# Kernel tuning notes

Hardware: AMD Instinct MI355X
Metric: run time of the kernel (lower is better)

Reference implementation:

```python
import jax, jax.numpy as jnp
import numpy as np

B, T, IN, H, L, P = 512, 512, 1, 100, 4, 0.5  # batch, seq, input, hidden, layers, dropout


def setup_inputs() -> dict:
    key = jax.random.key(0)
    ks = jax.random.split(key, 12)
    k = 1.0 / np.sqrt(H)  # torch nn.LSTM init scale
    u = lambda kk, shape: jax.random.uniform(kk, shape, jnp.float32, -k, k)
    inp = {
        "x": jax.random.normal(ks[0], (B, T, IN), jnp.float32),
        "W_ih0": u(ks[1], (4 * H, IN)),          # layer 0 input weights
        "W_ih_rest": u(ks[2], (L - 1, 4 * H, H)),  # layers 1..3 input weights
        "W_hh": u(ks[3], (L, 4 * H, H)),
        "b_ih": u(ks[4], (L, 4 * H)),
        "b_hh": u(ks[5], (L, 4 * H)),
        "W_out": u(ks[6], (1, H)),
        "b_out": u(ks[7], (1,)),
        # inter-layer dropout keep-masks (torch applies dropout to outputs of layers 0..L-2)
        "drop_masks": jax.random.bernoulli(ks[8], 1.0 - P, (L - 1, B, T, H)).astype(jnp.float32),
    }
    return inp


def _lstm_layer(seq, Wih, Whh, b):
    # seq: [T, B, in_dim]; returns [T, B, H]. PyTorch gate order: i, f, g, o.
    h0 = jnp.zeros((seq.shape[1], Whh.shape[-1]), seq.dtype)

    def step(carry, xt):
        h, c = carry
        gates = xt @ Wih.T + h @ Whh.T + b  # [B, 4H]
        i, f, g, o = jnp.split(gates, 4, axis=-1)
        c = jax.nn.sigmoid(f) * c + jax.nn.sigmoid(i) * jnp.tanh(g)
        h = jax.nn.sigmoid(o) * jnp.tanh(c)
        return (h, c), h

    _, hs = jax.lax.scan(step, (h0, h0), seq)
    return hs


def reference(x, W_ih0, W_ih_rest, W_hh, b_ih, b_hh, W_out, b_out, drop_masks):
    scale = 1.0 / (1.0 - P)
    seq = jnp.swapaxes(x, 0, 1)  # [T, B, IN] (batch_first -> time-major)
    seq = _lstm_layer(seq, W_ih0, W_hh[0], b_ih[0] + b_hh[0])
    for l in range(1, L):
        seq = seq * (jnp.swapaxes(drop_masks[l - 1], 0, 1) * scale)
        seq = _lstm_layer(seq, W_ih_rest[l - 1], W_hh[l], b_ih[l] + b_hh[l])
    last = seq[-1]  # [B, H] == lstm_out[:, -1]
    return last @ W_out.T + b_out  # [B, 1]
```

## Files before the change

kernel.cpp:

```cpp
#include <hip/hip_runtime.h>
#include <cstdint>
#include <cstddef>

#define BB 512
#define TT 512
#define HH 100
#define G4 400

template<bool IS_L0, bool WRITE_DROP>
__global__ __launch_bounds__(448, 2)
void rec_kernel(const float* __restrict__ x,
                const float* __restrict__ xc,
                const float* __restrict__ Whh_l,
                const float* __restrict__ Wih0,
                const float* __restrict__ bih_l,
                const float* __restrict__ bhh_l,
                const float* __restrict__ dmask_l,
                float* __restrict__ hdrop,
                float* __restrict__ st_h,
                float* __restrict__ st_c)
{
    __shared__ float hbuf[2][2][112];
    __shared__ float gsh[2][400];

    const int tid = threadIdx.x;
    const int p   = tid >> 1;
    const int e   = tid & 1;
    const bool rowok = (p < 200);
    const int pc  = rowok ? p : 199;
    const int r0  = pc;
    const int r1  = pc + 200;
    const int b   = blockIdx.x * 2 + e;

    float wf0[100], wf1[100];
    {
        const float4* w0 = (const float4*)(Whh_l + (size_t)r0 * HH);
        const float4* w1 = (const float4*)(Whh_l + (size_t)r1 * HH);
        #pragma unroll
        for (int m = 0; m < 25; ++m) {
            ((float4*)wf0)[m] = w0[m];
            ((float4*)wf1)[m] = w1[m];
        }
    }

    float wx0 = 0.f, wx1 = 0.f, bs0 = 0.f, bs1 = 0.f;
    if (IS_L0) {
        wx0 = Wih0[r0];  bs0 = bih_l[r0] + bhh_l[r0];
        wx1 = Wih0[r1];  bs1 = bih_l[r1] + bhh_l[r1];
    }

    ((float*)hbuf)[tid] = 0.f;

    const bool p2 = (p < HH);
    const int jj  = p2 ? p : 0;
    float c2 = 0.f, hlast = 0.f;

    __syncthreads();

    float gin0 = 0.f, gin1 = 0.f, xv = 0.f, mk = 0.f;
    if (IS_L0) {
        xv = x[(size_t)b * TT];
    } else {
        gin0 = xc[(size_t)b * G4 + r0];
        gin1 = xc[(size_t)b * G4 + r1];
    }
    if (WRITE_DROP && p2) mk = dmask_l[(size_t)b * TT * HH + jj];

    int cur = 0;
    for (int t = 0; t < TT; ++t) {
        const int tn = (t + 1 < TT) ? (t + 1) : t;

        float nxv = 0.f, ngin0 = 0.f, ngin1 = 0.f, nmk = 0.f;
        if (IS_L0) {
            nxv = x[(size_t)b * TT + tn];
        } else {
            const size_t base = (size_t)tn * BB * G4 + (size_t)b * G4;
            ngin0 = xc[base + r0];
            ngin1 = xc[base + r1];
        }
        if (WRITE_DROP && p2) nmk = dmask_l[((size_t)b * TT + tn) * HH + jj];

        if (IS_L0) {
            gin0 = fmaf(xv, wx0, bs0);
            gin1 = fmaf(xv, wx1, bs1);
        }

        float a0 = 0.f, a0b = 0.f, a1 = 0.f, a1b = 0.f;
        {
            const float4* hp = (const float4*)&hbuf[cur][e][0];
            #pragma unroll
            for (int m = 0; m < 25; ++m) {
                const float4 hv = hp[m];
                a0  = fmaf(wf0[4 * m + 0], hv.x, a0);
                a0b = fmaf(wf0[4 * m + 1], hv.y, a0b);
                a0  = fmaf(wf0[4 * m + 2], hv.z, a0);
                a0b = fmaf(wf0[4 * m + 3], hv.w, a0b);
                a1  = fmaf(wf1[4 * m + 0], hv.x, a1);
                a1b = fmaf(wf1[4 * m + 1], hv.y, a1b);
                a1  = fmaf(wf1[4 * m + 2], hv.z, a1);
                a1b = fmaf(wf1[4 * m + 3], hv.w, a1b);
            }
        }
        if (rowok) {
            gsh[e][pc]       = a0 + a0b + gin0;
            gsh[e][pc + 200] = a1 + a1b + gin1;
        }
        __syncthreads();

        const int nxt = cur ^ 1;
        if (p2) {
            const float gi = gsh[e][jj];
            const float gf = gsh[e][HH + jj];
            const float gg = gsh[e][2 * HH + jj];
            const float go = gsh[e][3 * HH + jj];
            const float i_ = 1.f / (1.f + __expf(-gi));
            const float f_ = 1.f / (1.f + __expf(-gf));
            const float o_ = 1.f / (1.f + __expf(-go));
            const float gt = 1.f - 2.f / (__expf(gg + gg) + 1.f);
            c2 = fmaf(f_, c2, i_ * gt);
            const float th = 1.f - 2.f / (__expf(c2 + c2) + 1.f);
            const float h = o_ * th;
            hlast = h;
            hbuf[nxt][e][jj] = h;
            if (WRITE_DROP)
                hdrop[((size_t)t * BB + b) * HH + jj] = h * mk * 2.f;
        }
        __syncthreads();
        cur = nxt;
        gin0 = ngin0; gin1 = ngin1;
        xv = nxv; mk = nmk;
    }

    if (p2) {
        st_h[(size_t)b * HH + jj] = hlast;
        st_c[(size_t)b * HH + jj] = c2;
    }
}

__global__ __launch_bounds__(256, 2)
void xc_gemm(const float* __restrict__ A,
             const float* __restrict__ W,
             const float* __restrict__ bih_l,
             const float* __restrict__ bhh_l,
             float* __restrict__ xc)
{
    __shared__ float At[HH][132];
    __shared__ float Bt[HH][68];

    const int tid = threadIdx.x;
    const int n0  = blockIdx.x * 64;
    const size_t m0 = (size_t)blockIdx.y * 128;

    for (int s = tid; s < 128 * 25; s += 256) {
        const int r = s / 25, kq = s - r * 25;
        const float4 v = *(const float4*)&A[(m0 + r) * HH + kq * 4];
        At[kq * 4 + 0][r] = v.x; At[kq * 4 + 1][r] = v.y;
        At[kq * 4 + 2][r] = v.z; At[kq * 4 + 3][r] = v.w;
    }
    for (int s = tid; s < 64 * 25; s += 256) {
        const int r = s / 25, kq = s - r * 25;
        const int col = n0 + r;
        float4 v = {0.f, 0.f, 0.f, 0.f};
        if (col < G4) v = *(const float4*)&W[(size_t)col * HH + kq * 4];
        Bt[kq * 4 + 0][r] = v.x; Bt[kq * 4 + 1][r] = v.y;
        Bt[kq * 4 + 2][r] = v.z; Bt[kq * 4 + 3][r] = v.w;
    }
    __syncthreads();

    const int tx = tid & 15;
    const int ty = tid >> 4;
    float acc[8][4];
    #pragma unroll
    for (int i = 0; i < 8; ++i)
        #pragma unroll
        for (int j = 0; j < 4; ++j) acc[i][j] = 0.f;

    #pragma unroll 4
    for (int k = 0; k < HH; ++k) {
        const float4 a0 = *(const float4*)&At[k][ty * 8];
        const float4 a1 = *(const float4*)&At[k][ty * 8 + 4];
        const float4 bv = *(const float4*)&Bt[k][tx * 4];
        const float av[8] = {a0.x, a0.y, a0.z, a0.w, a1.x, a1.y, a1.z, a1.w};
        #pragma unroll
        for (int i = 0; i < 8; ++i) {
            acc[i][0] = fmaf(av[i], bv.x, acc[i][0]);
            acc[i][1] = fmaf(av[i], bv.y, acc[i][1]);
            acc[i][2] = fmaf(av[i], bv.z, acc[i][2]);
            acc[i][3] = fmaf(av[i], bv.w, acc[i][3]);
        }
    }

    const int col = n0 + tx * 4;
    if (col < G4) {
        const float4 u = *(const float4*)&bih_l[col];
        const float4 v = *(const float4*)&bhh_l[col];
        const float4 bias = {u.x + v.x, u.y + v.y, u.z + v.z, u.w + v.w};
        #pragma unroll
        for (int i = 0; i < 8; ++i) {
            const size_t r = m0 + ty * 8 + i;
            float4 o = {acc[i][0] + bias.x, acc[i][1] + bias.y,
                        acc[i][2] + bias.z, acc[i][3] + bias.w};
            *(float4*)&xc[r * G4 + col] = o;
        }
    }
}

__global__ __launch_bounds__(256)
void out_kernel(const float* __restrict__ st_h3,
                const float* __restrict__ Wout,
                const float* __restrict__ bout,
                float* __restrict__ out)
{
    const int b = blockIdx.x * 256 + threadIdx.x;
    if (b < BB) {
        float sum = bout[0];
        #pragma unroll 4
        for (int k = 0; k < HH; ++k)
            sum = fmaf(st_h3[(size_t)b * HH + k], Wout[k], sum);
        out[b] = sum;
    }
}

extern "C" void kernel_launch(void* const* d_in, const int* in_sizes, int n_in,
                              void* d_out, int out_size, void* d_ws, size_t ws_size,
                              hipStream_t stream)
{
    const float* x     = (const float*)d_in[0];
    const float* Wih0  = (const float*)d_in[1];
    const float* WihR  = (const float*)d_in[2];
    const float* Whh   = (const float*)d_in[3];
    const float* bih   = (const float*)d_in[4];
    const float* bhh   = (const float*)d_in[5];
    const float* Wout  = (const float*)d_in[6];
    const float* bout  = (const float*)d_in[7];
    const float* dmask = (const float*)d_in[8];
    float* out = (float*)d_out;

    float* ws    = (float*)d_ws;
    float* xcb   = ws;
    float* hdrop = xcb + (size_t)TT * BB * G4;
    float* sth   = hdrop + (size_t)TT * BB * HH;
    float* stc   = sth + (size_t)4 * BB * HH;

    const dim3 rgrid(BB / 2), rblk(448);
    const dim3 ggrid(7, (TT * BB) / 128), gblk(256);

    rec_kernel<true, true><<<rgrid, rblk, 0, stream>>>(
        x, nullptr, Whh, Wih0, bih, bhh, dmask,
        hdrop, sth, stc);
    for (int l = 1; l < 4; ++l) {
        xc_gemm<<<ggrid, gblk, 0, stream>>>(
            hdrop, WihR + (size_t)(l - 1) * G4 * HH,
            bih + l * G4, bhh + l * G4, xcb);
        if (l < 3) {
            rec_kernel<false, true><<<rgrid, rblk, 0, stream>>>(
                nullptr, xcb, Whh + (size_t)l * G4 * HH,
                nullptr, nullptr, nullptr,
                dmask + (size_t)l * BB * TT * HH,
                hdrop, sth + (size_t)l * BB * HH, stc + (size_t)l * BB * HH);
        } else {
            rec_kernel<false, false><<<rgrid, rblk, 0, stream>>>(
                nullptr, xcb, Whh + (size_t)l * G4 * HH,
                nullptr, nullptr, nullptr,
                nullptr,
                nullptr, sth + (size_t)l * BB * HH, stc + (size_t)l * BB * HH);
        }
    }
    out_kernel<<<dim3(2), dim3(256), 0, stream>>>(sth + (size_t)3 * BB * HH, Wout, bout, out);
}
```

Measured before the change: 4.155 ms.

## Rework recurrent kernel activations and widen xc GEMM tile to 128x128

The recurrent kernel now stages the W_hh matrix through a 160KB shared buffer so the per-thread weight loads are coalesced, and drops its occupancy hint to one block per CU. It also moves gate activations (sigmoid, and tanh for the g gate) into the GEMV threads, so the cell-update threads only compute c and h. The input GEMM switches to a 128x128 tile with an 8x8 per-thread micro-tile and scalar staging loads, using fewer column blocks. The large shared allocation limits residency to one block per CU, and the scalar GEMM loads may coalesce less well.

After: 5.920 ms. 1.42x slower.

```diff
diff --git a/kernel.cpp b/kernel.cpp
--- a/kernel.cpp
+++ b/kernel.cpp
@@ -8,7 +8,7 @@
 #define G4 400
 
 template<bool IS_L0, bool WRITE_DROP>
-__global__ __launch_bounds__(448, 2)
+__global__ __launch_bounds__(448, 1)
 void rec_kernel(const float* __restrict__ x,
                 const float* __restrict__ xc,
                 const float* __restrict__ Whh_l,
@@ -20,8 +20,7 @@
                 float* __restrict__ st_h,
                 float* __restrict__ st_c)
 {
-    __shared__ float hbuf[2][2][112];
-    __shared__ float gsh[2][400];
+    __shared__ float sh[G4 * HH];
 
     const int tid = threadIdx.x;
     const int p   = tid >> 1;
@@ -32,16 +31,25 @@
     const int r1  = pc + 200;
     const int b   = blockIdx.x * 2 + e;
 
-    float wf0[100], wf1[100];
     {
-        const float4* w0 = (const float4*)(Whh_l + (size_t)r0 * HH);
-        const float4* w1 = (const float4*)(Whh_l + (size_t)r1 * HH);
+        const float4* src = (const float4*)Whh_l;
+        float4* dst = (float4*)sh;
+        for (int i = tid; i < G4 * HH / 4; i += 448) dst[i] = src[i];
+    }
+    __syncthreads();
+
+    float4 wf0[25], wf1[25];
+    {
+        const float4* s0 = (const float4*)&sh[r0 * HH];
+        const float4* s1 = (const float4*)&sh[r1 * HH];
         #pragma unroll
-        for (int m = 0; m < 25; ++m) {
-            ((float4*)wf0)[m] = w0[m];
-            ((float4*)wf1)[m] = w1[m];
-        }
-    }
+        for (int m = 0; m < 25; ++m) { wf0[m] = s0[m]; wf1[m] = s1[m]; }
+    }
+    __syncthreads();
+
+    for (int i = tid; i < G4 * HH; i += 448) sh[i] = 0.f;
+
+    float* gshp = sh + 448;
 
     float wx0 = 0.f, wx1 = 0.f, bs0 = 0.f, bs1 = 0.f;
     if (IS_L0) {
@@ -49,10 +57,9 @@
         wx1 = Wih0[r1];  bs1 = bih_l[r1] + bhh_l[r1];
     }
 
-    ((float*)hbuf)[tid] = 0.f;
-
-    const bool p2 = (p < HH);
-    const int jj  = p2 ? p : 0;
+    const bool isP2 = (tid < 200);
+    const int jj  = p;
+    const bool sel = (p < HH);
     float c2 = 0.f, hlast = 0.f;
 
     __syncthreads();
@@ -64,7 +71,7 @@
         gin0 = xc[(size_t)b * G4 + r0];
         gin1 = xc[(size_t)b * G4 + r1];
     }
-    if (WRITE_DROP && p2) mk = dmask_l[(size_t)b * TT * HH + jj];
+    if (WRITE_DROP && isP2) mk = dmask_l[(size_t)b * TT * HH + jj];
 
     int cur = 0;
     for (int t = 0; t < TT; ++t) {
@@ -74,11 +81,11 @@
         if (IS_L0) {
             nxv = x[(size_t)b * TT + tn];
         } else {
-            const size_t base = (size_t)tn * BB * G4 + (size_t)b * G4;
+            const size_t base = (size_t)tn * (BB * G4) + (size_t)b * G4;
             ngin0 = xc[base + r0];
             ngin1 = xc[base + r1];
         }
-        if (WRITE_DROP && p2) nmk = dmask_l[((size_t)b * TT + tn) * HH + jj];
+        if (WRITE_DROP && isP2) nmk = dmask_l[((size_t)b * TT + tn) * HH + jj];
 
         if (IS_L0) {
             gin0 = fmaf(xv, wx0, bs0);
@@ -87,57 +94,60 @@
 
         float a0 = 0.f, a0b = 0.f, a1 = 0.f, a1b = 0.f;
         {
-            const float4* hp = (const float4*)&hbuf[cur][e][0];
+            const float4* hp = (const float4*)&sh[cur * 224 + e * 112];
             #pragma unroll
             for (int m = 0; m < 25; ++m) {
                 const float4 hv = hp[m];
-                a0  = fmaf(wf0[4 * m + 0], hv.x, a0);
-                a0b = fmaf(wf0[4 * m + 1], hv.y, a0b);
-                a0  = fmaf(wf0[4 * m + 2], hv.z, a0);
-                a0b = fmaf(wf0[4 * m + 3], hv.w, a0b);
-                a1  = fmaf(wf1[4 * m + 0], hv.x, a1);
-                a1b = fmaf(wf1[4 * m + 1], hv.y, a1b);
-                a1  = fmaf(wf1[4 * m + 2], hv.z, a1);
-                a1b = fmaf(wf1[4 * m + 3], hv.w, a1b);
+                a0  = fmaf(wf0[m].x, hv.x, a0);
+                a0b = fmaf(wf0[m].y, hv.y, a0b);
+                a0  = fmaf(wf0[m].z, hv.z, a0);
+                a0b = fmaf(wf0[m].w, hv.w, a0b);
+                a1  = fmaf(wf1[m].x, hv.x, a1);
+                a1b = fmaf(wf1[m].y, hv.y, a1b);
+                a1  = fmaf(wf1[m].z, hv.z, a1);
+                a1b = fmaf(wf1[m].w, hv.w, a1b);
             }
         }
+        const float pre0 = a0 + a0b + gin0;
+        const float pre1 = a1 + a1b + gin1;
+        const float E0   = __expf(-pre0);
+        const float act0 = 1.f / (1.f + E0);
+        const float E1   = __expf(sel ? (pre1 + pre1) : (-pre1));
+        const float rr   = 1.f / (1.f + E1);
+        const float act1 = sel ? fmaf(-2.f, rr, 1.f) : rr;
         if (rowok) {
-            gsh[e][pc]       = a0 + a0b + gin0;
-            gsh[e][pc + 200] = a1 + a1b + gin1;
+            gshp[e * G4 + pc]       = act0;
+            gshp[e * G4 + pc + 200] = act1;
         }
         __syncthreads();
 
         const int nxt = cur ^ 1;
-        if (p2) {
-            const float gi = gsh[e][jj];
-            const float gf = gsh[e][HH + jj];
-            const float gg = gsh[e][2 * HH + jj];
-            const float go = gsh[e][3 * HH + jj];
-            const float i_ = 1.f / (1.f + __expf(-gi));
-            const float f_ = 1.f / (1.f + __expf(-gf));
-            const float o_ = 1.f / (1.f + __expf(-go));
-            const float gt = 1.f - 2.f / (__expf(gg + gg) + 1.f);
-            c2 = fmaf(f_, c2, i_ * gt);
-            const float th = 1.f - 2.f / (__expf(c2 + c2) + 1.f);
-            const float h = o_ * th;
+        if (isP2) {
+            const float i_ = gshp[e * G4 + jj];
+            const float f_ = gshp[e * G4 + 100 + jj];
+            const float g_ = gshp[e * G4 + 200 + jj];
+            const float o_ = gshp[e * G4 + 300 + jj];
+            c2 = fmaf(f_, c2, i_ * g_);
+            const float Ec = __expf(c2 + c2);
+            const float th = 1.f - 2.f / (Ec + 1.f);
+            const float h  = o_ * th;
             hlast = h;
-            hbuf[nxt][e][jj] = h;
+            sh[nxt * 224 + e * 112 + jj] = h;
             if (WRITE_DROP)
                 hdrop[((size_t)t * BB + b) * HH + jj] = h * mk * 2.f;
         }
         __syncthreads();
         cur = nxt;
-        gin0 = ngin0; gin1 = ngin1;
-        xv = nxv; mk = nmk;
-    }
-
-    if (p2) {
+        gin0 = ngin0; gin1 = ngin1; xv = nxv; mk = nmk;
+    }
+
+    if (isP2) {
         st_h[(size_t)b * HH + jj] = hlast;
         st_c[(size_t)b * HH + jj] = c2;
     }
 }
 
-__global__ __launch_bounds__(256, 2)
+__global__ __launch_bounds__(256)
 void xc_gemm(const float* __restrict__ A,
              const float* __restrict__ W,
              const float* __restrict__ bih_l,
@@ -145,62 +155,68 @@
              float* __restrict__ xc)
 {
     __shared__ float At[HH][132];
-    __shared__ float Bt[HH][68];
+    __shared__ float Bt[HH][132];
 
     const int tid = threadIdx.x;
-    const int n0  = blockIdx.x * 64;
+    const int n0  = blockIdx.x * 128;
     const size_t m0 = (size_t)blockIdx.y * 128;
 
-    for (int s = tid; s < 128 * 25; s += 256) {
-        const int r = s / 25, kq = s - r * 25;
-        const float4 v = *(const float4*)&A[(m0 + r) * HH + kq * 4];
-        At[kq * 4 + 0][r] = v.x; At[kq * 4 + 1][r] = v.y;
-        At[kq * 4 + 2][r] = v.z; At[kq * 4 + 3][r] = v.w;
-    }
-    for (int s = tid; s < 64 * 25; s += 256) {
-        const int r = s / 25, kq = s - r * 25;
+    for (int s = tid; s < 128 * HH; s += 256) {
+        const int r = s / HH, k = s - r * HH;
+        At[k][r] = A[(m0 + r) * HH + k];
         const int col = n0 + r;
-        float4 v = {0.f, 0.f, 0.f, 0.f};
-        if (col < G4) v = *(const float4*)&W[(size_t)col * HH + kq * 4];
-        Bt[kq * 4 + 0][r] = v.x; Bt[kq * 4 + 1][r] = v.y;
-        Bt[kq * 4 + 2][r] = v.z; Bt[kq * 4 + 3][r] = v.w;
-    }
-    __syncthreads();
-
-    const int tx = tid & 15;
-    const int ty = tid >> 4;
-    float acc[8][4];
+        Bt[k][r] = (col < G4) ? W[(size_t)col * HH + k] : 0.f;
+    }
+    __syncthreads();
+
+    const int tx = tid & 15, ty = tid >> 4;
+    float acc[8][8];
     #pragma unroll
     for (int i = 0; i < 8; ++i)
         #pragma unroll
-        for (int j = 0; j < 4; ++j) acc[i][j] = 0.f;
-
-    #pragma unroll 4
+        for (int j = 0; j < 8; ++j) acc[i][j] = 0.f;
+
+    #pragma unroll 2
     for (int k = 0; k < HH; ++k) {
-        const float4 a0 = *(const float4*)&At[k][ty * 8];
-        const float4 a1 = *(const float4*)&At[k][ty * 8 + 4];
-        const float4 bv = *(const float4*)&Bt[k][tx * 4];
+        const float4 a0 = *(const float4*)&At[k][ty * 4];
+        const float4 a1 = *(const float4*)&At[k][64 + ty * 4];
+        const float4 b0 = *(const float4*)&Bt[k][tx * 4];
+        const float4 b1 = *(const float4*)&Bt[k][64 + tx * 4];
         const float av[8] = {a0.x, a0.y, a0.z, a0.w, a1.x, a1.y, a1.z, a1.w};
+        const float bv[8] = {b0.x, b0.y, b0.z, b0.w, b1.x, b1.y, b1.z, b1.w};
         #pragma unroll
-        for (int i = 0; i < 8; ++i) {
-            acc[i][0] = fmaf(av[i], bv.x, acc[i][0]);
-            acc[i][1] = fmaf(av[i], bv.y, acc[i][1]);
-            acc[i][2] = fmaf(av[i], bv.z, acc[i][2]);
-            acc[i][3] = fmaf(av[i], bv.w, acc[i][3]);
-        }
-    }
-
-    const int col = n0 + tx * 4;
-    if (col < G4) {
-        const float4 u = *(const float4*)&bih_l[col];
-        const float4 v = *(const float4*)&bhh_l[col];
-        const float4 bias = {u.x + v.x, u.y + v.y, u.z + v.z, u.w + v.w};
-        #pragma unroll
-        for (int i = 0; i < 8; ++i) {
-            const size_t r = m0 + ty * 8 + i;
-            float4 o = {acc[i][0] + bias.x, acc[i][1] + bias.y,
-                        acc[i][2] + bias.z, acc[i][3] + bias.w};
-            *(float4*)&xc[r * G4 + col] = o;
+        for (int i = 0; i < 8; ++i)
+            #pragma unroll
+            for (int j = 0; j < 8; ++j)
+                acc[i][j] = fmaf(av[i], bv[j], acc[i][j]);
+    }
+
+    const int c0 = n0 + tx * 4;
+    const int c1 = n0 + 64 + tx * 4;
+    float4 biasA = {0,0,0,0}, biasB = {0,0,0,0};
+    if (c0 < G4) {
+        const float4 u = *(const float4*)&bih_l[c0];
+        const float4 v = *(const float4*)&bhh_l[c0];
+        biasA = {u.x + v.x, u.y + v.y, u.z + v.z, u.w + v.w};
+    }
+    if (c1 < G4) {
+        const float4 u = *(const float4*)&bih_l[c1];
+        const float4 v = *(const float4*)&bhh_l[c1];
+        biasB = {u.x + v.x, u.y + v.y, u.z + v.z, u.w + v.w};
+    }
+
+    #pragma unroll
+    for (int i = 0; i < 8; ++i) {
+        const size_t row = m0 + ((i < 4) ? ty * 4 + i : 64 + ty * 4 + (i - 4));
+        if (c0 < G4) {
+            float4 o = {acc[i][0] + biasA.x, acc[i][1] + biasA.y,
+                        acc[i][2] + biasA.z, acc[i][3] + biasA.w};
+            *(float4*)&xc[row * G4 + c0] = o;
+        }
+        if (c1 < G4) {
+            float4 o = {acc[i][4] + biasB.x, acc[i][5] + biasB.y,
+                        acc[i][6] + biasB.z, acc[i][7] + biasB.w};
+            *(float4*)&xc[row * G4 + c1] = o;
         }
     }
 }
@@ -243,7 +259,7 @@
     float* stc   = sth + (size_t)4 * BB * HH;
 
     const dim3 rgrid(BB / 2), rblk(448);
-    const dim3 ggrid(7, (TT * BB) / 128), gblk(256);
+    const dim3 ggrid(4, (TT * BB) / 128), gblk(256);
 
     rec_kernel<true, true><<<rgrid, rblk, 0, stream>>>(
         x, nullptr, Whh, Wih0, bih, bhh, dmask,
```
